# Kernel optimization log

Measured on AMD Instinct MI355X. Metric: run time of the kernel, lower is better.

## Reference

```python
import jax, jax.numpy as jnp
import numpy as np

E = 512   # fusion_dim
H = 8     # num_heads
HD = E // H
NC = 6

def _ln(x, g, b, eps=1e-5):
    m = jnp.mean(x, axis=-1, keepdims=True)
    v = jnp.mean((x - m) ** 2, axis=-1, keepdims=True)
    return (x - m) * jax.lax.rsqrt(v + eps) * g + b

def _lin(x, w, b):
    # torch nn.Linear: w is (out, in)
    return x @ w.T + b

def setup_inputs() -> dict:
    key = jax.random.key(0)
    ks = iter(jax.random.split(key, 32))
    B = 16384
    d = {
        'rgb':  jax.random.normal(next(ks), (B, 768), jnp.float32),
        'pose': jax.random.normal(next(ks), (B, 640), jnp.float32),
        'flow': jax.random.normal(next(ks), (B, 1024), jnp.float32),
    }
    def W(k, shape):
        return jax.random.normal(k, shape, jnp.float32) * 0.02
    # projection branches: Linear + LayerNorm
    d['rgb_w'] = W(next(ks), (E, 768));  d['rgb_b'] = jnp.zeros((E,))
    d['rgb_g'] = jnp.ones((E,));         d['rgb_beta'] = jnp.zeros((E,))
    d['pose_w'] = W(next(ks), (E, 640)); d['pose_b'] = jnp.zeros((E,))
    d['pose_g'] = jnp.ones((E,));        d['pose_beta'] = jnp.zeros((E,))
    d['flow_w'] = W(next(ks), (E, 1024)); d['flow_b'] = jnp.zeros((E,))
    d['flow_g'] = jnp.ones((E,));        d['flow_beta'] = jnp.zeros((E,))
    # MultiheadAttention packed qkv + out proj (torch layout)
    d['in_w'] = W(next(ks), (3 * E, E)); d['in_b'] = jnp.zeros((3 * E,))
    d['out_w'] = W(next(ks), (E, E));    d['out_b'] = jnp.zeros((E,))
    # gate MLP
    d['gw1'] = W(next(ks), (E, 3 * E)); d['gb1'] = jnp.zeros((E,))
    d['gw2'] = W(next(ks), (3, E));     d['gb2'] = jnp.zeros((3,))
    # classifier
    d['cw1'] = W(next(ks), (E // 2, E)); d['cb1'] = jnp.zeros((E // 2,))
    d['cg'] = jnp.ones((E // 2,));       d['cbeta'] = jnp.zeros((E // 2,))
    d['cw2'] = W(next(ks), (NC, E // 2)); d['cb2'] = jnp.zeros((NC,))
    return d

def _forward(rgb, pose, flow, rgb_w, rgb_b, rgb_g, rgb_beta,
             pose_w, pose_b, pose_g, pose_beta,
             flow_w, flow_b, flow_g, flow_beta,
             in_w, in_b, out_w, out_b,
             gw1, gb1, gw2, gb2,
             cw1, cb1, cg, cbeta, cw2, cb2):
    # per-modality projection: Linear -> LN -> ReLU (dropout = identity, eval mode)
    r = jax.nn.relu(_ln(_lin(rgb, rgb_w, rgb_b), rgb_g, rgb_beta))
    p = jax.nn.relu(_ln(_lin(pose, pose_w, pose_b), pose_g, pose_beta))
    f = jax.nn.relu(_ln(_lin(flow, flow_w, flow_b), flow_g, flow_beta))
    stacked = jnp.stack([r, p, f], axis=1)                 # (B, 3, E)
    # self-attention over the 3 modality tokens
    qkv = stacked @ in_w.T + in_b                          # (B, 3, 3E)
    q, k, v = jnp.split(qkv, 3, axis=-1)
    B = stacked.shape[0]
    q = q.reshape(B, 3, H, HD); k = k.reshape(B, 3, H, HD); v = v.reshape(B, 3, H, HD)
    scores = jnp.einsum('bqhd,bkhd->bhqk', q, k) / np.sqrt(HD).astype(np.float32)
    attn = jax.nn.softmax(scores, axis=-1)
    ctx = jnp.einsum('bhqk,bkhd->bqhd', attn, v).reshape(B, 3, E)
    attended = ctx @ out_w.T + out_b                       # (B, 3, E)
    # gating over concatenated projections
    concat = jnp.concatenate([r, p, f], axis=1)            # (B, 3E)
    gate = jax.nn.softmax(_lin(jax.nn.relu(_lin(concat, gw1, gb1)), gw2, gb2), axis=1)  # (B, 3)
    fused = jnp.einsum('bse,bs->be', attended, gate)       # (B, E)
    # classifier
    h = jax.nn.relu(_ln(_lin(fused, cw1, cb1), cg, cbeta))
    logits = _lin(h, cw2, cb2)                             # (B, NC)
    return logits, gate

def reference(rgb, pose, flow, rgb_w, rgb_b, rgb_g, rgb_beta,
              pose_w, pose_b, pose_g, pose_beta,
              flow_w, flow_b, flow_g, flow_beta,
              in_w, in_b, out_w, out_b,
              gw1, gb1, gw2, gb2,
              cw1, cb1, cg, cbeta, cw2, cb2):
    return _forward(rgb, pose, flow, rgb_w, rgb_b, rgb_g, rgb_beta,
                    pose_w, pose_b, pose_g, pose_beta,
                    flow_w, flow_b, flow_g, flow_beta,
                    in_w, in_b, out_w, out_b,
                    gw1, gb1, gw2, gb2,
                    cw1, cb1, cg, cbeta, cw2, cb2)
```

## Files before the change

### kernel.cpp

```cpp
#include <hip/hip_runtime.h>


typedef unsigned short u16;
typedef __bf16 bf16x8 __attribute__((ext_vector_type(8)));
typedef float f32x4  __attribute__((ext_vector_type(4)));
typedef unsigned short u16x8 __attribute__((ext_vector_type(8)));
typedef unsigned short u16x4 __attribute__((ext_vector_type(4)));

#define BATCH 16384

__device__ __forceinline__ u16 f2b(float f) {
  union { float f; unsigned int u; } c; c.f = f;
  unsigned int u = c.u;
  return (u16)((u + 0x7fffu + ((u >> 16) & 1u)) >> 16);
}
__device__ __forceinline__ float b2f(u16 h) {
  union { unsigned int u; float f; } c; c.u = ((unsigned int)h) << 16;
  return c.f;
}

struct CvtJobs {
  const float* s[7];
  u16* d[7];
  int n4[7];
};

__global__ __launch_bounds__(256) void cvt_w(CvtJobs J) {
  const int stride = gridDim.x * blockDim.x;
  const int tid = blockIdx.x * blockDim.x + threadIdx.x;
  for (int ji = 0; ji < 7; ++ji) {
    const f32x4* __restrict__ s = (const f32x4*)J.s[ji];
    u16x4* __restrict__ d = (u16x4*)J.d[ji];
    const int n4 = J.n4[ji];
    for (int i = tid; i < n4; i += stride) {
      f32x4 v = s[i];
      u16x4 o;
      #pragma unroll
      for (int c = 0; c < 4; ++c) o[c] = f2b(v[c]);
      d[i] = o;
    }
  }
}

template<int EPI>
__global__ __launch_bounds__(256) void gemm128(
    const u16* __restrict__ A, const u16* __restrict__ Bw,
    const float* __restrict__ bias, u16* __restrict__ C,
    int K, int ldc, int coff, int NB)
{
  __shared__ __align__(16) u16 As[2][4096];
  __shared__ __align__(16) u16 Bs[2][4096];
  const int id = blockIdx.x;
  const int rr = id & 7, jj = id >> 3;
  const int nb = jj % NB;
  const int mb = rr + ((jj / NB) << 3);
  const int m0 = mb << 7;
  const int n0 = nb << 7;

  const int t = threadIdx.x;
  const int wave = t >> 6, lane = t & 63;
  const int wm = wave & 1, wn = wave >> 1;
  const int lr  = lane & 15;
  const int lk8 = (lane >> 4) << 3;
  const int srow = t >> 2;
  const int scol = (t & 3) << 4;

  f32x4 acc[4][4] = {};

  const size_t rowB = (size_t)K * 2;
  const char* Ab = (const char*)A + (size_t)m0 * rowB + scol;
  const char* Bb = (const char*)Bw + (size_t)n0 * rowB + scol;

  auto stage = [&](int s, int buf) {
    const char* Ak = Ab + (size_t)s * 64;
    const char* Bk = Bb + (size_t)s * 64;
    #pragma unroll
    for (int j = 0; j < 2; ++j) {
      __builtin_amdgcn_global_load_lds(
          (const __attribute__((address_space(1))) void*)(Ak + (size_t)(j * 64 + srow) * rowB),
          (__attribute__((address_space(3))) void*)((char*)As[buf] + (j << 12) + (wave << 10)),
          16, 0, 0);
      __builtin_amdgcn_global_load_lds(
          (const __attribute__((address_space(1))) void*)(Bk + (size_t)(j * 64 + srow) * rowB),
          (__attribute__((address_space(3))) void*)((char*)Bs[buf] + (j << 12) + (wave << 10)),
          16, 0, 0);
    }
  };

  const int nsteps = K >> 5;
  stage(0, 0);
  for (int s = 0; s < nsteps; ++s) {
    const int cur = s & 1;
    __syncthreads();
    if (s + 1 < nsteps) stage(s + 1, cur ^ 1);

    bf16x8 af[4], bfr[4];
    #pragma unroll
    for (int mi = 0; mi < 4; ++mi) {
      const int r = (wm << 6) + (mi << 4) + lr;
      af[mi] = __builtin_bit_cast(bf16x8, *(const u16x8*)&As[cur][r * 32 + lk8]);
    }
    #pragma unroll
    for (int ni = 0; ni < 4; ++ni) {
      const int r = (wn << 6) + (ni << 4) + lr;
      bfr[ni] = __builtin_bit_cast(bf16x8, *(const u16x8*)&Bs[cur][r * 32 + lk8]);
    }
    #pragma unroll
    for (int mi = 0; mi < 4; ++mi)
      #pragma unroll
      for (int ni = 0; ni < 4; ++ni)
        acc[mi][ni] = __builtin_amdgcn_mfma_f32_16x16x32_bf16(
            af[mi], bfr[ni], acc[mi][ni], 0, 0, 0);
  }

  const int rquad = (lane >> 4) << 2;
  #pragma unroll
  for (int ni = 0; ni < 4; ++ni) {
    const int col = n0 + (wn << 6) + (ni << 4) + lr;
    const float bv = bias[col];
    #pragma unroll
    for (int mi = 0; mi < 4; ++mi) {
      const int rowb = m0 + (wm << 6) + (mi << 4) + rquad;
      #pragma unroll
      for (int r = 0; r < 4; ++r) {
        float v = acc[mi][ni][r] + bv;
        if (EPI == 2) v = fmaxf(v, 0.0f);
        C[(size_t)(rowb + r) * ldc + coff + col] = f2b(v);
      }
    }
  }
}

struct P3 {
  const float* A[3];
  const u16* W[3];
  const float* bias[3];
  int K[3];
  int coff[3];
  u16* C;
};

__global__ __launch_bounds__(256) void proj3_k(P3 p) {
  __shared__ __align__(16) u16 As[2][4096];
  __shared__ __align__(16) u16 Bs[2][4096];
  const int id = blockIdx.x;
  const int rr = id & 7, jj = id >> 3;
  const int nb = jj & 3;
  const int mz = rr + ((jj >> 2) << 3);
  const int mb = mz & 127;
  const int z  = mz >> 7;
  const int m0 = mb << 7;
  const int n0 = nb << 7;

  const float* __restrict__ A = p.A[z];
  const u16* __restrict__ Bw = p.W[z];
  const int K = p.K[z];

  const int t = threadIdx.x;
  const int wave = t >> 6, lane = t & 63;
  const int wm = wave & 1, wn = wave >> 1;
  const int lr  = lane & 15;
  const int lk8 = (lane >> 4) << 3;
  const int ar = t >> 3;
  const int ac = (t & 7) << 2;
  const int srow = t >> 2;
  const int scol = (t & 3) << 4;

  f32x4 acc[4][4] = {};

  const size_t rowA = (size_t)K;
  const size_t rowB = (size_t)K * 2;
  const float* Abase = A + (size_t)m0 * rowA + ac;
  const char* Bb = (const char*)Bw + (size_t)n0 * rowB + scol;

  f32x4 areg[4];
  auto loadA = [&](int s) {
    const float* Ak = Abase + s * 32;
    #pragma unroll
    for (int j = 0; j < 4; ++j)
      areg[j] = *(const f32x4*)(Ak + (size_t)(j * 32 + ar) * rowA);
  };
  auto writeA = [&](int buf) {
    #pragma unroll
    for (int j = 0; j < 4; ++j) {
      u16x4 o;
      #pragma unroll
      for (int c = 0; c < 4; ++c) o[c] = f2b(areg[j][c]);
      *(u16x4*)&As[buf][(j * 32 + ar) * 32 + ac] = o;
    }
  };
  auto stageB = [&](int s, int buf) {
    const char* Bk = Bb + (size_t)s * 64;
    #pragma unroll
    for (int j = 0; j < 2; ++j)
      __builtin_amdgcn_global_load_lds(
          (const __attribute__((address_space(1))) void*)(Bk + (size_t)(j * 64 + srow) * rowB),
          (__attribute__((address_space(3))) void*)((char*)Bs[buf] + (j << 12) + (wave << 10)),
          16, 0, 0);
  };

  const int nsteps = K >> 5;
  loadA(0);
  stageB(0, 0);
  writeA(0);
  for (int s = 0; s < nsteps; ++s) {
    const int cur = s & 1;
    __syncthreads();
    if (s + 1 < nsteps) { loadA(s + 1); stageB(s + 1, cur ^ 1); }

    bf16x8 af[4], bfr[4];
    #pragma unroll
    for (int mi = 0; mi < 4; ++mi) {
      const int r = (wm << 6) + (mi << 4) + lr;
      af[mi] = __builtin_bit_cast(bf16x8, *(const u16x8*)&As[cur][r * 32 + lk8]);
    }
    #pragma unroll
    for (int ni = 0; ni < 4; ++ni) {
      const int r = (wn << 6) + (ni << 4) + lr;
      bfr[ni] = __builtin_bit_cast(bf16x8, *(const u16x8*)&Bs[cur][r * 32 + lk8]);
    }
    #pragma unroll
    for (int mi = 0; mi < 4; ++mi)
      #pragma unroll
      for (int ni = 0; ni < 4; ++ni)
        acc[mi][ni] = __builtin_amdgcn_mfma_f32_16x16x32_bf16(
            af[mi], bfr[ni], acc[mi][ni], 0, 0, 0);

    if (s + 1 < nsteps) writeA(cur ^ 1);
  }

  const int rquad = (lane >> 4) << 2;
  #pragma unroll
  for (int ni = 0; ni < 4; ++ni) {
    const int col = n0 + (wn << 6) + (ni << 4) + lr;
    const float bv = p.bias[z][col];
    #pragma unroll
    for (int mi = 0; mi < 4; ++mi) {
      const int rowb = m0 + (wm << 6) + (mi << 4) + rquad;
      #pragma unroll
      for (int r = 0; r < 4; ++r) {
        p.C[(size_t)(rowb + r) * 1536 + p.coff[z] + col] = f2b(acc[mi][ni][r] + bv);
      }
    }
  }
}

__global__ __launch_bounds__(384) void ln3_k(
    const u16* __restrict__ raw, u16* __restrict__ dst,
    const float* __restrict__ g0, const float* __restrict__ b0,
    const float* __restrict__ g1, const float* __restrict__ b1,
    const float* __restrict__ g2, const float* __restrict__ b2)
{
  const int wave = threadIdx.x >> 6, lane = threadIdx.x & 63;
  const int m = wave % 3;
  const int b = blockIdx.x * 2 + wave / 3;
  const size_t off = (size_t)b * 1536 + m * 512 + lane * 8;
  u16x8 xa = *(const u16x8*)&raw[off];
  float x[8];
  float sum = 0.f, sq = 0.f;
  #pragma unroll
  for (int d = 0; d < 8; ++d) { float f = b2f(xa[d]); x[d] = f; sum += f; sq += f * f; }
  #pragma unroll
  for (int o = 32; o > 0; o >>= 1) { sum += __shfl_xor(sum, o); sq += __shfl_xor(sq, o); }
  const float mean = sum * (1.0f / 512.0f);
  const float var = sq * (1.0f / 512.0f) - mean * mean;
  const float rs = rsqrtf(var + 1e-5f);
  const float* g = (m == 0) ? g0 : (m == 1) ? g1 : g2;
  const float* bb = (m == 0) ? b0 : (m == 1) ? b1 : b2;
  u16x8 o;
  #pragma unroll
  for (int d = 0; d < 8; ++d) {
    float y = (x[d] - mean) * rs * g[lane * 8 + d] + bb[lane * 8 + d];
    o[d] = f2b(fmaxf(y, 0.0f));
  }
  *(u16x8*)&dst[off] = o;
}

template<int E>
__global__ __launch_bounds__(256) void ln_relu_k(
    const u16* __restrict__ src, u16* __restrict__ dst,
    const float* __restrict__ gg, const float* __restrict__ bb)
{
  constexpr int V = E >> 6;
  const int wave = threadIdx.x >> 6, lane = threadIdx.x & 63;
  const int row = blockIdx.x * 4 + wave;
  const u16* s = src + (size_t)row * E + lane * V;
  float x[V];
  float sum = 0.f, sq = 0.f;
  #pragma unroll
  for (int i = 0; i < V; i += 4) {
    u16x4 v = *(const u16x4*)(s + i);
    #pragma unroll
    for (int c = 0; c < 4; ++c) { float f = b2f(v[c]); x[i + c] = f; sum += f; sq += f * f; }
  }
  #pragma unroll
  for (int off = 32; off > 0; off >>= 1) {
    sum += __shfl_xor(sum, off);
    sq  += __shfl_xor(sq,  off);
  }
  const float invE = 1.0f / (float)E;
  const float m = sum * invE;
  const float var = sq * invE - m * m;
  const float rs = rsqrtf(var + 1e-5f);
  u16* d = dst + (size_t)row * E + lane * V;
  const float* g = gg + lane * V;
  const float* b = bb + lane * V;
  #pragma unroll
  for (int i = 0; i < V; i += 4) {
    u16x4 o;
    #pragma unroll
    for (int c = 0; c < 4; ++c) {
      float y = (x[i + c] - m) * rs * g[i + c] + b[i + c];
      o[c] = f2b(fmaxf(y, 0.0f));
    }
    *(u16x4*)(d + i) = o;
  }
}

__global__ __launch_bounds__(256) void gate2_k(
    const u16* __restrict__ gateh, const float* __restrict__ gw2,
    const float* __restrict__ gb2, float* __restrict__ gate_out)
{
  const int wave = threadIdx.x >> 6, lane = threadIdx.x & 63;
  const int b = blockIdx.x * 4 + wave;
  float x[8];
  u16x8 xa = *(const u16x8*)&gateh[(size_t)b * 512 + lane * 8];
  #pragma unroll
  for (int d = 0; d < 8; ++d) x[d] = b2f(xa[d]);
  float s[3] = {0.f, 0.f, 0.f};
  #pragma unroll
  for (int j = 0; j < 3; ++j) {
    const float* w = gw2 + j * 512 + lane * 8;
    #pragma unroll
    for (int d = 0; d < 8; ++d) s[j] += x[d] * w[d];
  }
  #pragma unroll
  for (int m = 1; m < 64; m <<= 1)
    #pragma unroll
    for (int j = 0; j < 3; ++j) s[j] += __shfl_xor(s[j], m);
  if (lane == 0) {
    #pragma unroll
    for (int j = 0; j < 3; ++j) s[j] += gb2[j];
    const float mx = fmaxf(s[0], fmaxf(s[1], s[2]));
    float e0 = __expf(s[0] - mx), e1 = __expf(s[1] - mx), e2 = __expf(s[2] - mx);
    const float inv = 1.0f / (e0 + e1 + e2);
    gate_out[b * 3 + 0] = e0 * inv;
    gate_out[b * 3 + 1] = e1 * inv;
    gate_out[b * 3 + 2] = e2 * inv;
  }
}

__global__ __launch_bounds__(256) void attn_gate_k(
    const u16* __restrict__ qkv, const float* __restrict__ gate,
    u16* __restrict__ ctxg, int b0)
{
  const int gid = blockIdx.x * 256 + threadIdx.x;
  const int b = gid >> 6;
  const int h = (threadIdx.x >> 3) & 7;
  const int ld = threadIdx.x & 7;
  const size_t rb = (size_t)(3 * b) * 1536 + h * 64 + ld * 8;

  float q[3][8], k[3][8], v[3][8];
  #pragma unroll
  for (int i = 0; i < 3; ++i) {
    u16x8 qa = *(const u16x8*)&qkv[rb + (size_t)i * 1536];
    u16x8 ka = *(const u16x8*)&qkv[rb + (size_t)i * 1536 + 512];
    u16x8 va = *(const u16x8*)&qkv[rb + (size_t)i * 1536 + 1024];
    #pragma unroll
    for (int d = 0; d < 8; ++d) { q[i][d] = b2f(qa[d]); k[i][d] = b2f(ka[d]); v[i][d] = b2f(va[d]); }
  }
  float s[9];
  #pragma unroll
  for (int i = 0; i < 3; ++i)
    #pragma unroll
    for (int j = 0; j < 3; ++j) {
      float a = 0.f;
      #pragma unroll
      for (int d = 0; d < 8; ++d) a += q[i][d] * k[j][d];
      s[i * 3 + j] = a;
    }
  #pragma unroll
  for (int m = 1; m < 8; m <<= 1)
    #pragma unroll
    for (int e = 0; e < 9; ++e) s[e] += __shfl_xor(s[e], m);

  const float g0 = gate[(size_t)(b0 + b) * 3 + 0];
  const float g1 = gate[(size_t)(b0 + b) * 3 + 1];
  const float g2 = gate[(size_t)(b0 + b) * 3 + 2];
  const float gg[3] = {g0, g1, g2};

  float o[8] = {};
  const float sc = 0.125f;
  #pragma unroll
  for (int i = 0; i < 3; ++i) {
    const float a0 = s[i * 3 + 0] * sc, a1 = s[i * 3 + 1] * sc, a2 = s[i * 3 + 2] * sc;
    const float mx = fmaxf(a0, fmaxf(a1, a2));
    float e0 = __expf(a0 - mx), e1 = __expf(a1 - mx), e2 = __expf(a2 - mx);
    const float inv = gg[i] / (e0 + e1 + e2);
    e0 *= inv; e1 *= inv; e2 *= inv;
    #pragma unroll
    for (int d = 0; d < 8; ++d)
      o[d] += e0 * v[0][d] + e1 * v[1][d] + e2 * v[2][d];
  }
  u16x8 ov;
  #pragma unroll
  for (int d = 0; d < 8; ++d) ov[d] = f2b(o[d]);
  *(u16x8*)&ctxg[(size_t)(b0 + b) * 512 + h * 64 + ld * 8] = ov;
}

__global__ __launch_bounds__(256) void cls2_k(
    const u16* __restrict__ hh, const float* __restrict__ cw2,
    const float* __restrict__ cb2, float* __restrict__ logits)
{
  const int wave = threadIdx.x >> 6, lane = threadIdx.x & 63;
  const int b = blockIdx.x * 4 + wave;
  float x[4];
  u16x4 xa = *(const u16x4*)&hh[(size_t)b * 256 + lane * 4];
  #pragma unroll
  for (int d = 0; d < 4; ++d) x[d] = b2f(xa[d]);
  float s[6] = {};
  #pragma unroll
  for (int j = 0; j < 6; ++j) {
    const float* w = cw2 + j * 256 + lane * 4;
    #pragma unroll
    for (int d = 0; d < 4; ++d) s[j] += x[d] * w[d];
  }
  #pragma unroll
  for (int m = 1; m < 64; m <<= 1)
    #pragma unroll
    for (int j = 0; j < 6; ++j) s[j] += __shfl_xor(s[j], m);
  if (lane < 6) logits[(size_t)b * 6 + lane] = s[lane] + cb2[lane];
}

extern "C" void kernel_launch(void* const* d_in, const int* in_sizes, int n_in,
                              void* d_out, int out_size, void* d_ws, size_t ws_size,
                              hipStream_t stream) {
  const float* rgb       = (const float*)d_in[0];
  const float* pose      = (const float*)d_in[1];
  const float* flow      = (const float*)d_in[2];
  const float* rgb_w     = (const float*)d_in[3];
  const float* rgb_b     = (const float*)d_in[4];
  const float* rgb_g     = (const float*)d_in[5];
  const float* rgb_beta  = (const float*)d_in[6];
  const float* pose_w    = (const float*)d_in[7];
  const float* pose_b    = (const float*)d_in[8];
  const float* pose_g    = (const float*)d_in[9];
  const float* pose_beta = (const float*)d_in[10];
  const float* flow_w    = (const float*)d_in[11];
  const float* flow_b    = (const float*)d_in[12];
  const float* flow_g    = (const float*)d_in[13];
  const float* flow_beta = (const float*)d_in[14];
  const float* in_w      = (const float*)d_in[15];
  const float* in_b      = (const float*)d_in[16];
  const float* out_w     = (const float*)d_in[17];
  const float* out_b     = (const float*)d_in[18];
  const float* gw1       = (const float*)d_in[19];
  const float* gb1       = (const float*)d_in[20];
  const float* gw2       = (const float*)d_in[21];
  const float* gb2       = (const float*)d_in[22];
  const float* cw1       = (const float*)d_in[23];
  const float* cb1       = (const float*)d_in[24];
  const float* cg        = (const float*)d_in[25];
  const float* cbeta     = (const float*)d_in[26];
  const float* cw2       = (const float*)d_in[27];
  const float* cb2       = (const float*)d_in[28];

  float* logits_out = (float*)d_out;
  float* gate_out   = (float*)d_out + (size_t)BATCH * 6;

  char* ws = (char*)d_ws;
  u16* w_rgb  = (u16*)(ws + 0);
  u16* w_pose = (u16*)(ws + 786432);
  u16* w_flow = (u16*)(ws + 1441792);
  u16* w_in   = (u16*)(ws + 2490368);
  u16* w_out  = (u16*)(ws + 4063232);
  u16* w_g1   = (u16*)(ws + 4587520);
  u16* w_c1   = (u16*)(ws + 6160384);
  char* rpfB = ws + 6422528;
  char* B2   = ws + 56754176;
  char* Cb   = ws + 132251648;
  char* Db   = ws + 149028864;

  u16*   rpf      = (u16*)rpfB;
  u16*   raw      = (u16*)B2;
  u16*   qkv_buf  = (u16*)B2;
  u16*   gateh    = (u16*)Cb;
  u16*   fusedb   = (u16*)Cb;
  u16*   ctxg     = (u16*)Db;
  u16*   cls_tmp  = (u16*)Db;
  u16*   h_bf     = (u16*)(Db + 8388608);

  CvtJobs J;
  const float* srcs[7] = {rgb_w, pose_w, flow_w, in_w, out_w, gw1, cw1};
  u16* dsts[7] = {w_rgb, w_pose, w_flow, w_in, w_out, w_g1, w_c1};
  int ns[7] = {512 * 768, 512 * 640, 512 * 1024, 1536 * 512, 512 * 512, 512 * 1536, 256 * 512};
  for (int i = 0; i < 7; ++i) { J.s[i] = srcs[i]; J.d[i] = dsts[i]; J.n4[i] = ns[i] / 4; }
  cvt_w<<<128, 256, 0, stream>>>(J);

  dim3 blk(256);
  P3 p;
  p.A[0] = rgb;  p.W[0] = w_rgb;  p.bias[0] = rgb_b;  p.K[0] = 768;  p.coff[0] = 0;
  p.A[1] = pose; p.W[1] = w_pose; p.bias[1] = pose_b; p.K[1] = 640;  p.coff[1] = 512;
  p.A[2] = flow; p.W[2] = w_flow; p.bias[2] = flow_b; p.K[2] = 1024; p.coff[2] = 1024;
  p.C = raw;
  proj3_k<<<1536, blk, 0, stream>>>(p);
  ln3_k<<<BATCH / 2, dim3(384), 0, stream>>>(raw, rpf, rgb_g, rgb_beta, pose_g, pose_beta, flow_g, flow_beta);

  gemm128<2><<<4 * (BATCH / 128), blk, 0, stream>>>(rpf, w_g1, gb1, gateh, 1536, 512, 0, 4);
  gate2_k<<<BATCH / 4, blk, 0, stream>>>(gateh, gw2, gb2, gate_out);

  for (int c = 0; c < 2; ++c) {
    const u16* a_chunk = rpf + (size_t)c * 8192 * 1536;
    gemm128<1><<<12 * (3 * 8192 / 128), blk, 0, stream>>>(
        a_chunk, w_in, in_b, qkv_buf, 512, 1536, 0, 12);
    attn_gate_k<<<8192 / 4, blk, 0, stream>>>(qkv_buf, gate_out, ctxg, c * 8192);
  }

  gemm128<1><<<4 * (BATCH / 128), blk, 0, stream>>>(ctxg, w_out, out_b, fusedb, 512, 512, 0, 4);

  gemm128<1><<<2 * (BATCH / 128), blk, 0, stream>>>(fusedb, w_c1, cb1, cls_tmp, 512, 256, 0, 2);
  ln_relu_k<256><<<BATCH / 4, blk, 0, stream>>>(cls_tmp, h_bf, cg, cbeta);
  cls2_k<<<BATCH / 4, blk, 0, stream>>>(h_bf, cw2, cb2, logits_out);

  (void)in_sizes; (void)n_in; (void)out_size; (void)ws_size;
}
```

Before: 549.7 us.

## Drop LDS staging in GEMMs; load MFMA fragments directly from global memory

Both the generic bf16 GEMM and the fused fp32-input projection GEMM stop staging tiles through shared memory. Each wave now loads its MFMA operand fragments straight from global memory into registers, double-buffered two k-steps deep, and converts fp32 to bf16 in registers for the projection. This removes the LDS writes and reads and the per-step block barriers. In exchange, waves in the same block no longer share tiles, so global and L2 traffic per block rises. Each lane also issues 16-byte loads strided by the row length, which coalesces poorly.

```diff
diff --git a/kernel.cpp b/kernel.cpp
--- a/kernel.cpp
+++ b/kernel.cpp
@@ -17,6 +17,12 @@
 __device__ __forceinline__ float b2f(u16 h) {
   union { unsigned int u; float f; } c; c.u = ((unsigned int)h) << 16;
   return c.f;
+}
+__device__ __forceinline__ bf16x8 cvt8(f32x4 lo, f32x4 hi) {
+  bf16x8 v;
+  #pragma unroll
+  for (int d = 0; d < 4; ++d) { v[d] = (__bf16)lo[d]; v[4 + d] = (__bf16)hi[d]; }
+  return v;
 }
 
 struct CvtJobs {
@@ -43,74 +49,65 @@
 }
 
 template<int EPI>
-__global__ __launch_bounds__(256) void gemm128(
+__global__ __launch_bounds__(256) void gemm_d(
     const u16* __restrict__ A, const u16* __restrict__ Bw,
     const float* __restrict__ bias, u16* __restrict__ C,
     int K, int ldc, int coff, int NB)
 {
-  __shared__ __align__(16) u16 As[2][4096];
-  __shared__ __align__(16) u16 Bs[2][4096];
   const int id = blockIdx.x;
   const int rr = id & 7, jj = id >> 3;
   const int nb = jj % NB;
   const int mb = rr + ((jj / NB) << 3);
-  const int m0 = mb << 7;
-  const int n0 = nb << 7;
+  const int m0 = mb << 7, n0 = nb << 7;
 
   const int t = threadIdx.x;
   const int wave = t >> 6, lane = t & 63;
   const int wm = wave & 1, wn = wave >> 1;
   const int lr  = lane & 15;
   const int lk8 = (lane >> 4) << 3;
-  const int srow = t >> 2;
-  const int scol = (t & 3) << 4;
 
   f32x4 acc[4][4] = {};
 
-  const size_t rowB = (size_t)K * 2;
-  const char* Ab = (const char*)A + (size_t)m0 * rowB + scol;
-  const char* Bb = (const char*)Bw + (size_t)n0 * rowB + scol;
-
-  auto stage = [&](int s, int buf) {
-    const char* Ak = Ab + (size_t)s * 64;
-    const char* Bk = Bb + (size_t)s * 64;
-    #pragma unroll
-    for (int j = 0; j < 2; ++j) {
-      __builtin_amdgcn_global_load_lds(
-          (const __attribute__((address_space(1))) void*)(Ak + (size_t)(j * 64 + srow) * rowB),
-          (__attribute__((address_space(3))) void*)((char*)As[buf] + (j << 12) + (wave << 10)),
-          16, 0, 0);
-      __builtin_amdgcn_global_load_lds(
-          (const __attribute__((address_space(1))) void*)(Bk + (size_t)(j * 64 + srow) * rowB),
-          (__attribute__((address_space(3))) void*)((char*)Bs[buf] + (j << 12) + (wave << 10)),
-          16, 0, 0);
-    }
-  };
+  const u16* ap[4];
+  const u16* bp[4];
+  #pragma unroll
+  for (int i = 0; i < 4; ++i) {
+    ap[i] = A  + (size_t)(m0 + (wm << 6) + (i << 4) + lr) * K + lk8;
+    bp[i] = Bw + (size_t)(n0 + (wn << 6) + (i << 4) + lr) * K + lk8;
+  }
+
+  u16x8 a0[4], b0[4], a1[4], b1[4];
+  #pragma unroll
+  for (int i = 0; i < 4; ++i) { a0[i] = *(const u16x8*)ap[i]; b0[i] = *(const u16x8*)bp[i]; }
 
   const int nsteps = K >> 5;
-  stage(0, 0);
-  for (int s = 0; s < nsteps; ++s) {
-    const int cur = s & 1;
-    __syncthreads();
-    if (s + 1 < nsteps) stage(s + 1, cur ^ 1);
-
-    bf16x8 af[4], bfr[4];
-    #pragma unroll
-    for (int mi = 0; mi < 4; ++mi) {
-      const int r = (wm << 6) + (mi << 4) + lr;
-      af[mi] = __builtin_bit_cast(bf16x8, *(const u16x8*)&As[cur][r * 32 + lk8]);
-    }
-    #pragma unroll
-    for (int ni = 0; ni < 4; ++ni) {
-      const int r = (wn << 6) + (ni << 4) + lr;
-      bfr[ni] = __builtin_bit_cast(bf16x8, *(const u16x8*)&Bs[cur][r * 32 + lk8]);
+  for (int s = 0; s < nsteps; s += 2) {
+    #pragma unroll
+    for (int i = 0; i < 4; ++i) {
+      a1[i] = *(const u16x8*)(ap[i] + (s + 1) * 32);
+      b1[i] = *(const u16x8*)(bp[i] + (s + 1) * 32);
     }
     #pragma unroll
     for (int mi = 0; mi < 4; ++mi)
       #pragma unroll
       for (int ni = 0; ni < 4; ++ni)
         acc[mi][ni] = __builtin_amdgcn_mfma_f32_16x16x32_bf16(
-            af[mi], bfr[ni], acc[mi][ni], 0, 0, 0);
+            __builtin_bit_cast(bf16x8, a0[mi]), __builtin_bit_cast(bf16x8, b0[ni]),
+            acc[mi][ni], 0, 0, 0);
+    if (s + 2 < nsteps) {
+      #pragma unroll
+      for (int i = 0; i < 4; ++i) {
+        a0[i] = *(const u16x8*)(ap[i] + (s + 2) * 32);
+        b0[i] = *(const u16x8*)(bp[i] + (s + 2) * 32);
+      }
+    }
+    #pragma unroll
+    for (int mi = 0; mi < 4; ++mi)
+      #pragma unroll
+      for (int ni = 0; ni < 4; ++ni)
+        acc[mi][ni] = __builtin_amdgcn_mfma_f32_16x16x32_bf16(
+            __builtin_bit_cast(bf16x8, a1[mi]), __builtin_bit_cast(bf16x8, b1[ni]),
+            acc[mi][ni], 0, 0, 0);
   }
 
   const int rquad = (lane >> 4) << 2;
@@ -141,16 +138,13 @@
 };
 
 __global__ __launch_bounds__(256) void proj3_k(P3 p) {
-  __shared__ __align__(16) u16 As[2][4096];
-  __shared__ __align__(16) u16 Bs[2][4096];
   const int id = blockIdx.x;
   const int rr = id & 7, jj = id >> 3;
   const int nb = jj & 3;
   const int mz = rr + ((jj >> 2) << 3);
   const int mb = mz & 127;
   const int z  = mz >> 7;
-  const int m0 = mb << 7;
-  const int n0 = nb << 7;
+  const int m0 = mb << 7, n0 = nb << 7;
 
   const float* __restrict__ A = p.A[z];
   const u16* __restrict__ Bw = p.W[z];
@@ -161,72 +155,60 @@
   const int wm = wave & 1, wn = wave >> 1;
   const int lr  = lane & 15;
   const int lk8 = (lane >> 4) << 3;
-  const int ar = t >> 3;
-  const int ac = (t & 7) << 2;
-  const int srow = t >> 2;
-  const int scol = (t & 3) << 4;
 
   f32x4 acc[4][4] = {};
 
-  const size_t rowA = (size_t)K;
-  const size_t rowB = (size_t)K * 2;
-  const float* Abase = A + (size_t)m0 * rowA + ac;
-  const char* Bb = (const char*)Bw + (size_t)n0 * rowB + scol;
-
-  f32x4 areg[4];
-  auto loadA = [&](int s) {
-    const float* Ak = Abase + s * 32;
-    #pragma unroll
-    for (int j = 0; j < 4; ++j)
-      areg[j] = *(const f32x4*)(Ak + (size_t)(j * 32 + ar) * rowA);
-  };
-  auto writeA = [&](int buf) {
-    #pragma unroll
-    for (int j = 0; j < 4; ++j) {
-      u16x4 o;
-      #pragma unroll
-      for (int c = 0; c < 4; ++c) o[c] = f2b(areg[j][c]);
-      *(u16x4*)&As[buf][(j * 32 + ar) * 32 + ac] = o;
-    }
-  };
-  auto stageB = [&](int s, int buf) {
-    const char* Bk = Bb + (size_t)s * 64;
-    #pragma unroll
-    for (int j = 0; j < 2; ++j)
-      __builtin_amdgcn_global_load_lds(
-          (const __attribute__((address_space(1))) void*)(Bk + (size_t)(j * 64 + srow) * rowB),
-          (__attribute__((address_space(3))) void*)((char*)Bs[buf] + (j << 12) + (wave << 10)),
-          16, 0, 0);
-  };
+  const float* ap[4];
+  const u16* bp[4];
+  #pragma unroll
+  for (int i = 0; i < 4; ++i) {
+    ap[i] = A  + (size_t)(m0 + (wm << 6) + (i << 4) + lr) * K + lk8;
+    bp[i] = Bw + (size_t)(n0 + (wn << 6) + (i << 4) + lr) * K + lk8;
+  }
+
+  f32x4 alo0[4], ahi0[4], alo1[4], ahi1[4];
+  u16x8 b0[4], b1[4];
+  #pragma unroll
+  for (int i = 0; i < 4; ++i) {
+    alo0[i] = *(const f32x4*)ap[i];
+    ahi0[i] = *(const f32x4*)(ap[i] + 4);
+    b0[i]   = *(const u16x8*)bp[i];
+  }
 
   const int nsteps = K >> 5;
-  loadA(0);
-  stageB(0, 0);
-  writeA(0);
-  for (int s = 0; s < nsteps; ++s) {
-    const int cur = s & 1;
-    __syncthreads();
-    if (s + 1 < nsteps) { loadA(s + 1); stageB(s + 1, cur ^ 1); }
-
-    bf16x8 af[4], bfr[4];
+  for (int s = 0; s < nsteps; s += 2) {
+    #pragma unroll
+    for (int i = 0; i < 4; ++i) {
+      const float* q = ap[i] + (s + 1) * 32;
+      alo1[i] = *(const f32x4*)q;
+      ahi1[i] = *(const f32x4*)(q + 4);
+      b1[i]   = *(const u16x8*)(bp[i] + (s + 1) * 32);
+    }
     #pragma unroll
     for (int mi = 0; mi < 4; ++mi) {
-      const int r = (wm << 6) + (mi << 4) + lr;
-      af[mi] = __builtin_bit_cast(bf16x8, *(const u16x8*)&As[cur][r * 32 + lk8]);
-    }
-    #pragma unroll
-    for (int ni = 0; ni < 4; ++ni) {
-      const int r = (wn << 6) + (ni << 4) + lr;
-      bfr[ni] = __builtin_bit_cast(bf16x8, *(const u16x8*)&Bs[cur][r * 32 + lk8]);
-    }
-    #pragma unroll
-    for (int mi = 0; mi < 4; ++mi)
+      const bf16x8 af = cvt8(alo0[mi], ahi0[mi]);
       #pragma unroll
       for (int ni = 0; ni < 4; ++ni)
         acc[mi][ni] = __builtin_amdgcn_mfma_f32_16x16x32_bf16(
-            af[mi], bfr[ni], acc[mi][ni], 0, 0, 0);
-
-    if (s + 1 < nsteps) writeA(cur ^ 1);
+            af, __builtin_bit_cast(bf16x8, b0[ni]), acc[mi][ni], 0, 0, 0);
+    }
+    if (s + 2 < nsteps) {
+      #pragma unroll
+      for (int i = 0; i < 4; ++i) {
+        const float* q = ap[i] + (s + 2) * 32;
+        alo0[i] = *(const f32x4*)q;
+        ahi0[i] = *(const f32x4*)(q + 4);
+        b0[i]   = *(const u16x8*)(bp[i] + (s + 2) * 32);
+      }
+    }
+    #pragma unroll
+    for (int mi = 0; mi < 4; ++mi) {
+      const bf16x8 af = cvt8(alo1[mi], ahi1[mi]);
+      #pragma unroll
+      for (int ni = 0; ni < 4; ++ni)
+        acc[mi][ni] = __builtin_amdgcn_mfma_f32_16x16x32_bf16(
+            af, __builtin_bit_cast(bf16x8, b1[ni]), acc[mi][ni], 0, 0, 0);
+    }
   }
 
   const int rquad = (lane >> 4) << 2;
@@ -506,19 +488,19 @@
   proj3_k<<<1536, blk, 0, stream>>>(p);
   ln3_k<<<BATCH / 2, dim3(384), 0, stream>>>(raw, rpf, rgb_g, rgb_beta, pose_g, pose_beta, flow_g, flow_beta);
 
-  gemm128<2><<<4 * (BATCH / 128), blk, 0, stream>>>(rpf, w_g1, gb1, gateh, 1536, 512, 0, 4);
+  gemm_d<2><<<4 * (BATCH / 128), blk, 0, stream>>>(rpf, w_g1, gb1, gateh, 1536, 512, 0, 4);
   gate2_k<<<BATCH / 4, blk, 0, stream>>>(gateh, gw2, gb2, gate_out);
 
   for (int c = 0; c < 2; ++c) {
     const u16* a_chunk = rpf + (size_t)c * 8192 * 1536;
-    gemm128<1><<<12 * (3 * 8192 / 128), blk, 0, stream>>>(
+    gemm_d<1><<<12 * (3 * 8192 / 128), blk, 0, stream>>>(
         a_chunk, w_in, in_b, qkv_buf, 512, 1536, 0, 12);
     attn_gate_k<<<8192 / 4, blk, 0, stream>>>(qkv_buf, gate_out, ctxg, c * 8192);
   }
 
-  gemm128<1><<<4 * (BATCH / 128), blk, 0, stream>>>(ctxg, w_out, out_b, fusedb, 512, 512, 0, 4);
-
-  gemm128<1><<<2 * (BATCH / 128), blk, 0, stream>>>(fusedb, w_c1, cb1, cls_tmp, 512, 256, 0, 2);
+  gemm_d<1><<<4 * (BATCH / 128), blk, 0, stream>>>(ctxg, w_out, out_b, fusedb, 512, 512, 0, 4);
+
+  gemm_d<1><<<2 * (BATCH / 128), blk, 0, stream>>>(fusedb, w_c1, cb1, cls_tmp, 512, 256, 0, 2);
   ln_relu_k<256><<<BATCH / 4, blk, 0, stream>>>(cls_tmp, h_bf, cg, cbeta);
   cls2_k<<<BATCH / 4, blk, 0, stream>>>(h_bf, cw2, cb2, logits_out);
 
```

After: 903.3 us. +64.3%, slower.

## Merge gate GEMM with first QKV chunk, fuse gate softmax and classifier tail

Applied to the files above, without the earlier changes.

The gate MLP's first GEMM now runs in the same multi-job launch as the first-chunk QKV projection, so the two GEMMs share one grid. The gate second layer and softmax move into the attention kernel, and the classifier LayerNorm, ReLU and final linear become a single tail kernel. This removes several launches and intermediate round-trips through global memory. The GEMM epilogue ReLU changes from a template parameter to a runtime flag, which adds a small per-element branch.

```diff
diff --git a/kernel.cpp b/kernel.cpp
--- a/kernel.cpp
+++ b/kernel.cpp
@@ -42,21 +42,12 @@
   }
 }
 
-template<int EPI>
-__global__ __launch_bounds__(256) void gemm128(
+__device__ __forceinline__ void gemm_body(
     const u16* __restrict__ A, const u16* __restrict__ Bw,
     const float* __restrict__ bias, u16* __restrict__ C,
-    int K, int ldc, int coff, int NB)
+    int K, int ldc, int coff, int relu, int m0, int n0,
+    u16 (*As)[4096], u16 (*Bs)[4096])
 {
-  __shared__ __align__(16) u16 As[2][4096];
-  __shared__ __align__(16) u16 Bs[2][4096];
-  const int id = blockIdx.x;
-  const int rr = id & 7, jj = id >> 3;
-  const int nb = jj % NB;
-  const int mb = rr + ((jj / NB) << 3);
-  const int m0 = mb << 7;
-  const int n0 = nb << 7;
-
   const int t = threadIdx.x;
   const int wave = t >> 6, lane = t & 63;
   const int wm = wave & 1, wn = wave >> 1;
@@ -124,125 +115,41 @@
       #pragma unroll
       for (int r = 0; r < 4; ++r) {
         float v = acc[mi][ni][r] + bv;
-        if (EPI == 2) v = fmaxf(v, 0.0f);
+        if (relu) v = fmaxf(v, 0.0f);
         C[(size_t)(rowb + r) * ldc + coff + col] = f2b(v);
       }
     }
   }
 }
 
-struct P3 {
-  const float* A[3];
-  const u16* W[3];
-  const float* bias[3];
-  int K[3];
-  int coff[3];
-  u16* C;
-};
-
-__global__ __launch_bounds__(256) void proj3_k(P3 p) {
+__global__ __launch_bounds__(256) void gemm128(
+    const u16* __restrict__ A, const u16* __restrict__ Bw,
+    const float* __restrict__ bias, u16* __restrict__ C,
+    int K, int ldc, int coff, int NB, int relu)
+{
   __shared__ __align__(16) u16 As[2][4096];
   __shared__ __align__(16) u16 Bs[2][4096];
   const int id = blockIdx.x;
   const int rr = id & 7, jj = id >> 3;
-  const int nb = jj & 3;
-  const int mz = rr + ((jj >> 2) << 3);
-  const int mb = mz & 127;
-  const int z  = mz >> 7;
-  const int m0 = mb << 7;
-  const int n0 = nb << 7;
-
-  const float* __restrict__ A = p.A[z];
-  const u16* __restrict__ Bw = p.W[z];
-  const int K = p.K[z];
-
-  const int t = threadIdx.x;
-  const int wave = t >> 6, lane = t & 63;
-  const int wm = wave & 1, wn = wave >> 1;
-  const int lr  = lane & 15;
-  const int lk8 = (lane >> 4) << 3;
-  const int ar = t >> 3;
-  const int ac = (t & 7) << 2;
-  const int srow = t >> 2;
-  const int scol = (t & 3) << 4;
-
-  f32x4 acc[4][4] = {};
-
-  const size_t rowA = (size_t)K;
-  const size_t rowB = (size_t)K * 2;
-  const float* Abase = A + (size_t)m0 * rowA + ac;
-  const char* Bb = (const char*)Bw + (size_t)n0 * rowB + scol;
-
-  f32x4 areg[4];
-  auto loadA = [&](int s) {
-    const float* Ak = Abase + s * 32;
-    #pragma unroll
-    for (int j = 0; j < 4; ++j)
-      areg[j] = *(const f32x4*)(Ak + (size_t)(j * 32 + ar) * rowA);
-  };
-  auto writeA = [&](int buf) {
-    #pragma unroll
-    for (int j = 0; j < 4; ++j) {
-      u16x4 o;
-      #pragma unroll
-      for (int c = 0; c < 4; ++c) o[c] = f2b(areg[j][c]);
-      *(u16x4*)&As[buf][(j * 32 + ar) * 32 + ac] = o;
-    }
-  };
-  auto stageB = [&](int s, int buf) {
-    const char* Bk = Bb + (size_t)s * 64;
-    #pragma unroll
-    for (int j = 0; j < 2; ++j)
-      __builtin_amdgcn_global_load_lds(
-          (const __attribute__((address_space(1))) void*)(Bk + (size_t)(j * 64 + srow) * rowB),
-          (__attribute__((address_space(3))) void*)((char*)Bs[buf] + (j << 12) + (wave << 10)),
-          16, 0, 0);
-  };
-
-  const int nsteps = K >> 5;
-  loadA(0);
-  stageB(0, 0);
-  writeA(0);
-  for (int s = 0; s < nsteps; ++s) {
-    const int cur = s & 1;
-    __syncthreads();
-    if (s + 1 < nsteps) { loadA(s + 1); stageB(s + 1, cur ^ 1); }
-
-    bf16x8 af[4], bfr[4];
-    #pragma unroll
-    for (int mi = 0; mi < 4; ++mi) {
-      const int r = (wm << 6) + (mi << 4) + lr;
-      af[mi] = __builtin_bit_cast(bf16x8, *(const u16x8*)&As[cur][r * 32 + lk8]);
-    }
-    #pragma unroll
-    for (int ni = 0; ni < 4; ++ni) {
-      const int r = (wn << 6) + (ni << 4) + lr;
-      bfr[ni] = __builtin_bit_cast(bf16x8, *(const u16x8*)&Bs[cur][r * 32 + lk8]);
-    }
-    #pragma unroll
-    for (int mi = 0; mi < 4; ++mi)
-      #pragma unroll
-      for (int ni = 0; ni < 4; ++ni)
-        acc[mi][ni] = __builtin_amdgcn_mfma_f32_16x16x32_bf16(
-            af[mi], bfr[ni], acc[mi][ni], 0, 0, 0);
-
-    if (s + 1 < nsteps) writeA(cur ^ 1);
-  }
-
-  const int rquad = (lane >> 4) << 2;
-  #pragma unroll
-  for (int ni = 0; ni < 4; ++ni) {
-    const int col = n0 + (wn << 6) + (ni << 4) + lr;
-    const float bv = p.bias[z][col];
-    #pragma unroll
-    for (int mi = 0; mi < 4; ++mi) {
-      const int rowb = m0 + (wm << 6) + (mi << 4) + rquad;
-      #pragma unroll
-      for (int r = 0; r < 4; ++r) {
-        p.C[(size_t)(rowb + r) * 1536 + p.coff[z] + col] = f2b(acc[mi][ni][r] + bv);
-      }
-    }
-  }
+  const int nb = jj % NB;
+  const int mb = rr + ((jj / NB) << 3);
+  gemm_body(A, Bw, bias, C, K, ldc, coff, relu, mb << 7, nb << 7, As, Bs);
+}
+
+struct GJob {
+  const u16* A; const u16* Bw; const float* bias; u16* C;
+  int K, ldc, coff, NB, relu;
+};
+__global__ __launch_bounds__(256) void gemm_mj(GJob j0, GJob j1, int split) {
+  __shared__ __align__(16) u16 As[2][4096];
+  __shared__ __align__(16) u16 Bs[2][4096];
+  GJob j = (blockIdx.x < split) ? j0 : j1;
+  const int id = (blockIdx.x < split) ? blockIdx.x : (blockIdx.x - split);
+  const int rr = id & 7, jj = id >> 3;
+  const int nb = jj % j.NB;
+  const int mb = rr + ((jj / j.NB) << 3);
+  gemm_body(j.A, j.Bw, j.bias, j.C, j.K, j.ldc, j.coff, j.relu,
+            mb << 7, nb << 7, As, Bs);
 }
 
 __global__ __launch_bounds__(384) void ln3_k(
@@ -276,90 +183,46 @@
   *(u16x8*)&dst[off] = o;
 }
 
-template<int E>
-__global__ __launch_bounds__(256) void ln_relu_k(
-    const u16* __restrict__ src, u16* __restrict__ dst,
-    const float* __restrict__ gg, const float* __restrict__ bb)
+__global__ __launch_bounds__(256) void attn_gate_k(
+    const u16* __restrict__ qkv, const u16* __restrict__ gateh,
+    const float* __restrict__ gw2, const float* __restrict__ gb2,
+    float* __restrict__ gate_out, u16* __restrict__ ctxg, int b0)
 {
-  constexpr int V = E >> 6;
-  const int wave = threadIdx.x >> 6, lane = threadIdx.x & 63;
-  const int row = blockIdx.x * 4 + wave;
-  const u16* s = src + (size_t)row * E + lane * V;
-  float x[V];
-  float sum = 0.f, sq = 0.f;
-  #pragma unroll
-  for (int i = 0; i < V; i += 4) {
-    u16x4 v = *(const u16x4*)(s + i);
-    #pragma unroll
-    for (int c = 0; c < 4; ++c) { float f = b2f(v[c]); x[i + c] = f; sum += f; sq += f * f; }
-  }
-  #pragma unroll
-  for (int off = 32; off > 0; off >>= 1) {
-    sum += __shfl_xor(sum, off);
-    sq  += __shfl_xor(sq,  off);
-  }
-  const float invE = 1.0f / (float)E;
-  const float m = sum * invE;
-  const float var = sq * invE - m * m;
-  const float rs = rsqrtf(var + 1e-5f);
-  u16* d = dst + (size_t)row * E + lane * V;
-  const float* g = gg + lane * V;
-  const float* b = bb + lane * V;
-  #pragma unroll
-  for (int i = 0; i < V; i += 4) {
-    u16x4 o;
-    #pragma unroll
-    for (int c = 0; c < 4; ++c) {
-      float y = (x[i + c] - m) * rs * g[i + c] + b[i + c];
-      o[c] = f2b(fmaxf(y, 0.0f));
-    }
-    *(u16x4*)(d + i) = o;
-  }
-}
-
-__global__ __launch_bounds__(256) void gate2_k(
-    const u16* __restrict__ gateh, const float* __restrict__ gw2,
-    const float* __restrict__ gb2, float* __restrict__ gate_out)
-{
-  const int wave = threadIdx.x >> 6, lane = threadIdx.x & 63;
+  const int wave = threadIdx.x >> 6;
+  const int lane = threadIdx.x & 63;
   const int b = blockIdx.x * 4 + wave;
-  float x[8];
-  u16x8 xa = *(const u16x8*)&gateh[(size_t)b * 512 + lane * 8];
-  #pragma unroll
-  for (int d = 0; d < 8; ++d) x[d] = b2f(xa[d]);
-  float s[3] = {0.f, 0.f, 0.f};
+  const int h = (lane >> 3) & 7;
+  const int ld = lane & 7;
+
+  float gx[8];
+  u16x8 ga = *(const u16x8*)&gateh[(size_t)(b0 + b) * 512 + lane * 8];
+  #pragma unroll
+  for (int d = 0; d < 8; ++d) gx[d] = b2f(ga[d]);
+  float s3[3] = {0.f, 0.f, 0.f};
   #pragma unroll
   for (int j = 0; j < 3; ++j) {
     const float* w = gw2 + j * 512 + lane * 8;
     #pragma unroll
-    for (int d = 0; d < 8; ++d) s[j] += x[d] * w[d];
+    for (int d = 0; d < 8; ++d) s3[j] += gx[d] * w[d];
   }
   #pragma unroll
   for (int m = 1; m < 64; m <<= 1)
     #pragma unroll
-    for (int j = 0; j < 3; ++j) s[j] += __shfl_xor(s[j], m);
+    for (int j = 0; j < 3; ++j) s3[j] += __shfl_xor(s3[j], m);
+  #pragma unroll
+  for (int j = 0; j < 3; ++j) s3[j] += gb2[j];
+  const float gmx = fmaxf(s3[0], fmaxf(s3[1], s3[2]));
+  float g0 = __expf(s3[0] - gmx), g1 = __expf(s3[1] - gmx), g2 = __expf(s3[2] - gmx);
+  const float ginv = 1.0f / (g0 + g1 + g2);
+  g0 *= ginv; g1 *= ginv; g2 *= ginv;
   if (lane == 0) {
-    #pragma unroll
-    for (int j = 0; j < 3; ++j) s[j] += gb2[j];
-    const float mx = fmaxf(s[0], fmaxf(s[1], s[2]));
-    float e0 = __expf(s[0] - mx), e1 = __expf(s[1] - mx), e2 = __expf(s[2] - mx);
-    const float inv = 1.0f / (e0 + e1 + e2);
-    gate_out[b * 3 + 0] = e0 * inv;
-    gate_out[b * 3 + 1] = e1 * inv;
-    gate_out[b * 3 + 2] = e2 * inv;
-  }
-}
-
-__global__ __launch_bounds__(256) void attn_gate_k(
-    const u16* __restrict__ qkv, const float* __restrict__ gate,
-    u16* __restrict__ ctxg, int b0)
-{
-  const int gid = blockIdx.x * 256 + threadIdx.x;
-  const int b = gid >> 6;
-  const int h = (threadIdx.x >> 3) & 7;
-  const int ld = threadIdx.x & 7;
+    gate_out[(size_t)(b0 + b) * 3 + 0] = g0;
+    gate_out[(size_t)(b0 + b) * 3 + 1] = g1;
+    gate_out[(size_t)(b0 + b) * 3 + 2] = g2;
+  }
+  const float gg[3] = {g0, g1, g2};
+
   const size_t rb = (size_t)(3 * b) * 1536 + h * 64 + ld * 8;
-
   float q[3][8], k[3][8], v[3][8];
   #pragma unroll
   for (int i = 0; i < 3; ++i) {
@@ -383,11 +246,6 @@
   for (int m = 1; m < 8; m <<= 1)
     #pragma unroll
     for (int e = 0; e < 9; ++e) s[e] += __shfl_xor(s[e], m);
-
-  const float g0 = gate[(size_t)(b0 + b) * 3 + 0];
-  const float g1 = gate[(size_t)(b0 + b) * 3 + 1];
-  const float g2 = gate[(size_t)(b0 + b) * 3 + 2];
-  const float gg[3] = {g0, g1, g2};
 
   float o[8] = {};
   const float sc = 0.125f;
@@ -408,28 +266,154 @@
   *(u16x8*)&ctxg[(size_t)(b0 + b) * 512 + h * 64 + ld * 8] = ov;
 }
 
-__global__ __launch_bounds__(256) void cls2_k(
-    const u16* __restrict__ hh, const float* __restrict__ cw2,
+__global__ __launch_bounds__(256) void cls_tail_k(
+    const u16* __restrict__ cls_tmp, const float* __restrict__ cg,
+    const float* __restrict__ cbeta, const float* __restrict__ cw2,
     const float* __restrict__ cb2, float* __restrict__ logits)
 {
   const int wave = threadIdx.x >> 6, lane = threadIdx.x & 63;
   const int b = blockIdx.x * 4 + wave;
   float x[4];
-  u16x4 xa = *(const u16x4*)&hh[(size_t)b * 256 + lane * 4];
-  #pragma unroll
-  for (int d = 0; d < 4; ++d) x[d] = b2f(xa[d]);
+  u16x4 xa = *(const u16x4*)&cls_tmp[(size_t)b * 256 + lane * 4];
+  float sum = 0.f, sq = 0.f;
+  #pragma unroll
+  for (int d = 0; d < 4; ++d) { float f = b2f(xa[d]); x[d] = f; sum += f; sq += f * f; }
+  #pragma unroll
+  for (int m = 32; m > 0; m >>= 1) { sum += __shfl_xor(sum, m); sq += __shfl_xor(sq, m); }
+  const float mean = sum * (1.0f / 256.0f);
+  const float var = sq * (1.0f / 256.0f) - mean * mean;
+  const float rs = rsqrtf(var + 1e-5f);
+  float h[4];
+  #pragma unroll
+  for (int d = 0; d < 4; ++d) {
+    const int c = lane * 4 + d;
+    h[d] = fmaxf((x[d] - mean) * rs * cg[c] + cbeta[c], 0.0f);
+  }
   float s[6] = {};
   #pragma unroll
   for (int j = 0; j < 6; ++j) {
     const float* w = cw2 + j * 256 + lane * 4;
     #pragma unroll
-    for (int d = 0; d < 4; ++d) s[j] += x[d] * w[d];
+    for (int d = 0; d < 4; ++d) s[j] += h[d] * w[d];
   }
   #pragma unroll
   for (int m = 1; m < 64; m <<= 1)
     #pragma unroll
     for (int j = 0; j < 6; ++j) s[j] += __shfl_xor(s[j], m);
   if (lane < 6) logits[(size_t)b * 6 + lane] = s[lane] + cb2[lane];
+}
+
+struct P3 {
+  const float* A[3];
+  const u16* W[3];
+  const float* bias[3];
+  int K[3];
+  int coff[3];
+  u16* C;
+};
+
+__global__ __launch_bounds__(256) void proj3_k(P3 p) {
+  __shared__ __align__(16) u16 As[2][4096];
+  __shared__ __align__(16) u16 Bs[2][4096];
+  const int id = blockIdx.x;
+  const int rr = id & 7, jj = id >> 3;
+  const int nb = jj & 3;
+  const int mz = rr + ((jj >> 2) << 3);
+  const int mb = mz & 127;
+  const int z  = mz >> 7;
+  const int m0 = mb << 7, n0 = nb << 7;
+
+  const float* __restrict__ A = p.A[z];
+  const u16* __restrict__ Bw = p.W[z];
+  const int K = p.K[z];
+
+  const int t = threadIdx.x;
+  const int wave = t >> 6, lane = t & 63;
+  const int wm = wave & 1, wn = wave >> 1;
+  const int lr  = lane & 15;
+  const int lk8 = (lane >> 4) << 3;
+  const int ar = t >> 3;
+  const int ac = (t & 7) << 2;
+  const int srow = t >> 2;
+  const int scol = (t & 3) << 4;
+
+  f32x4 acc[4][4] = {};
+
+  const size_t rowA = (size_t)K;
+  const size_t rowB = (size_t)K * 2;
+  const float* Abase = A + (size_t)m0 * rowA + ac;
+  const char* Bb = (const char*)Bw + (size_t)n0 * rowB + scol;
+
+  f32x4 areg[4];
+  auto loadA = [&](int s) {
+    const float* Ak = Abase + s * 32;
+    #pragma unroll
+    for (int j = 0; j < 4; ++j)
+      areg[j] = *(const f32x4*)(Ak + (size_t)(j * 32 + ar) * rowA);
+  };
+  auto writeA = [&](int buf) {
+    #pragma unroll
+    for (int j = 0; j < 4; ++j) {
+      u16x4 o;
+      #pragma unroll
+      for (int c = 0; c < 4; ++c) o[c] = f2b(areg[j][c]);
+      *(u16x4*)&As[buf][(j * 32 + ar) * 32 + ac] = o;
+    }
+  };
+  auto stageB = [&](int s, int buf) {
+    const char* Bk = Bb + (size_t)s * 64;
+    #pragma unroll
+    for (int j = 0; j < 2; ++j)
+      __builtin_amdgcn_global_load_lds(
+          (const __attribute__((address_space(1))) void*)(Bk + (size_t)(j * 64 + srow) * rowB),
+          (__attribute__((address_space(3))) void*)((char*)Bs[buf] + (j << 12) + (wave << 10)),
+          16, 0, 0);
+  };
+
+  const int nsteps = K >> 5;
+  loadA(0);
+  stageB(0, 0);
+  writeA(0);
+  for (int s = 0; s < nsteps; ++s) {
+    const int cur = s & 1;
+    __syncthreads();
+    if (s + 1 < nsteps) { loadA(s + 1); stageB(s + 1, cur ^ 1); }
+
+    bf16x8 af[4], bfr[4];
+    #pragma unroll
+    for (int mi = 0; mi < 4; ++mi) {
+      const int r = (wm << 6) + (mi << 4) + lr;
+      af[mi] = __builtin_bit_cast(bf16x8, *(const u16x8*)&As[cur][r * 32 + lk8]);
+    }
+    #pragma unroll
+    for (int ni = 0; ni < 4; ++ni) {
+      const int r = (wn << 6) + (ni << 4) + lr;
+      bfr[ni] = __builtin_bit_cast(bf16x8, *(const u16x8*)&Bs[cur][r * 32 + lk8]);
+    }
+    #pragma unroll
+    for (int mi = 0; mi < 4; ++mi)
+      #pragma unroll
+      for (int ni = 0; ni < 4; ++ni)
+        acc[mi][ni] = __builtin_amdgcn_mfma_f32_16x16x32_bf16(
+            af[mi], bfr[ni], acc[mi][ni], 0, 0, 0);
+
+    if (s + 1 < nsteps) writeA(cur ^ 1);
+  }
+
+  const int rquad = (lane >> 4) << 2;
+  #pragma unroll
+  for (int ni = 0; ni < 4; ++ni) {
+    const int col = n0 + (wn << 6) + (ni << 4) + lr;
+    const float bv = p.bias[z][col];
+    #pragma unroll
+    for (int mi = 0; mi < 4; ++mi) {
+      const int rowb = m0 + (wm << 6) + (mi << 4) + rquad;
+      #pragma unroll
+      for (int r = 0; r < 4; ++r) {
+        p.C[(size_t)(rowb + r) * 1536 + p.coff[z] + col] = f2b(acc[mi][ni][r] + bv);
+      }
+    }
+  }
 }
 
 extern "C" void kernel_launch(void* const* d_in, const int* in_sizes, int n_in,
@@ -476,19 +460,13 @@
   u16* w_out  = (u16*)(ws + 4063232);
   u16* w_g1   = (u16*)(ws + 4587520);
   u16* w_c1   = (u16*)(ws + 6160384);
-  char* rpfB = ws + 6422528;
-  char* B2   = ws + 56754176;
-  char* Cb   = ws + 132251648;
-  char* Db   = ws + 149028864;
-
-  u16*   rpf      = (u16*)rpfB;
-  u16*   raw      = (u16*)B2;
-  u16*   qkv_buf  = (u16*)B2;
-  u16*   gateh    = (u16*)Cb;
-  u16*   fusedb   = (u16*)Cb;
-  u16*   ctxg     = (u16*)Db;
-  u16*   cls_tmp  = (u16*)Db;
-  u16*   h_bf     = (u16*)(Db + 8388608);
+  u16* rpf     = (u16*)(ws + 6422528);
+  u16* raw     = (u16*)(ws + 56754176);
+  u16* qkv_buf = (u16*)(ws + 56754176);
+  u16* gateh   = (u16*)(ws + 132251648);
+  u16* fusedb  = (u16*)(ws + 132251648);
+  u16* ctxg    = (u16*)(ws + 149028864);
+  u16* cls_tmp = (u16*)(ws + 149028864);
 
   CvtJobs J;
   const float* srcs[7] = {rgb_w, pose_w, flow_w, in_w, out_w, gw1, cw1};
@@ -506,21 +484,23 @@
   proj3_k<<<1536, blk, 0, stream>>>(p);
   ln3_k<<<BATCH / 2, dim3(384), 0, stream>>>(raw, rpf, rgb_g, rgb_beta, pose_g, pose_beta, flow_g, flow_beta);
 
-  gemm128<2><<<4 * (BATCH / 128), blk, 0, stream>>>(rpf, w_g1, gb1, gateh, 1536, 512, 0, 4);
-  gate2_k<<<BATCH / 4, blk, 0, stream>>>(gateh, gw2, gb2, gate_out);
-
-  for (int c = 0; c < 2; ++c) {
-    const u16* a_chunk = rpf + (size_t)c * 8192 * 1536;
-    gemm128<1><<<12 * (3 * 8192 / 128), blk, 0, stream>>>(
-        a_chunk, w_in, in_b, qkv_buf, 512, 1536, 0, 12);
-    attn_gate_k<<<8192 / 4, blk, 0, stream>>>(qkv_buf, gate_out, ctxg, c * 8192);
-  }
-
-  gemm128<1><<<4 * (BATCH / 128), blk, 0, stream>>>(ctxg, w_out, out_b, fusedb, 512, 512, 0, 4);
-
-  gemm128<1><<<2 * (BATCH / 128), blk, 0, stream>>>(fusedb, w_c1, cb1, cls_tmp, 512, 256, 0, 2);
-  ln_relu_k<256><<<BATCH / 4, blk, 0, stream>>>(cls_tmp, h_bf, cg, cbeta);
-  cls2_k<<<BATCH / 4, blk, 0, stream>>>(h_bf, cw2, cb2, logits_out);
+  GJob jq, jg;
+  jq.A = rpf;                 jq.Bw = w_in; jq.bias = in_b; jq.C = qkv_buf;
+  jq.K = 512;  jq.ldc = 1536; jq.coff = 0; jq.NB = 12; jq.relu = 0;
+  jg.A = rpf;                 jg.Bw = w_g1; jg.bias = gb1; jg.C = gateh;
+  jg.K = 1536; jg.ldc = 512;  jg.coff = 0; jg.NB = 4;  jg.relu = 1;
+  gemm_mj<<<2304 + 512, blk, 0, stream>>>(jq, jg, 2304);
+
+  attn_gate_k<<<8192 / 4, blk, 0, stream>>>(qkv_buf, gateh, gw2, gb2, gate_out, ctxg, 0);
+
+  gemm128<<<2304, blk, 0, stream>>>(rpf + (size_t)8192 * 1536, w_in, in_b, qkv_buf,
+                                    512, 1536, 0, 12, 0);
+  attn_gate_k<<<8192 / 4, blk, 0, stream>>>(qkv_buf, gateh, gw2, gb2, gate_out, ctxg, 8192);
+
+  gemm128<<<512, blk, 0, stream>>>(ctxg, w_out, out_b, fusedb, 512, 512, 0, 4, 0);
+
+  gemm128<<<256, blk, 0, stream>>>(fusedb, w_c1, cb1, cls_tmp, 512, 256, 0, 2, 0);
+  cls_tail_k<<<BATCH / 4, blk, 0, stream>>>(cls_tmp, cg, cbeta, cw2, cb2, logits_out);
 
   (void)in_sizes; (void)n_in; (void)out_size; (void)ws_size;
 }
```

Result: no change. 552.0 us (+0.4%).
